# Optimization experiments

Measured on AMD Instinct MI355X. Metric: run time of the kernel, lower is better.

The kernel has to match this reference:

```python
import jax, jax.numpy as jnp
import numpy as np

B, C, L = 8, 256, 2048
D = C // 8  # q/k channel dim = 32


def setup_inputs() -> dict:
    key = jax.random.key(0)
    kx, kq, kk, kv, kg = jax.random.split(key, 5)
    kq1, kq2 = jax.random.split(kq)
    kk1, kk2 = jax.random.split(kk)
    kv1, kv2 = jax.random.split(kv)
    s = 0.05
    return {
        "x": jax.random.normal(kx, (B, C, L), dtype=jnp.float32),
        "Wq": jax.random.normal(kq1, (D, C), dtype=jnp.float32) * s,
        "bq": jax.random.normal(kq2, (D,), dtype=jnp.float32) * s,
        "Wk": jax.random.normal(kk1, (D, C), dtype=jnp.float32) * s,
        "bk": jax.random.normal(kk2, (D,), dtype=jnp.float32) * s,
        "Wv": jax.random.normal(kv1, (C, C), dtype=jnp.float32) * s,
        "bv": jax.random.normal(kv2, (C,), dtype=jnp.float32) * s,
        "gamma": jax.random.normal(kg, (1,), dtype=jnp.float32) * 0.1,
    }


def reference(x, Wq, bq, Wk, bk, Wv, bv, gamma):
    # 1x1 Conv1d == per-position channel matmul
    Q = jnp.einsum("dc,bcl->bld", Wq, x) + bq            # (B, L, D)
    K = jnp.einsum("dc,bcl->bdl", Wk, x) + bk[:, None]   # (B, D, L)
    V = jnp.einsum("oc,bcl->bol", Wv, x) + bv[:, None]   # (B, C, L)
    scale = jnp.float32(1.0 / np.sqrt(D))
    # attn[b, i, j]: softmax over j (keys)
    attn = jax.nn.softmax(jnp.einsum("bid,bdj->bij", Q, K) * scale, axis=-1)
    # out = V @ attn^T : out[b, c, i] = sum_j V[b, c, j] * attn[b, i, j]
    out = jnp.einsum("bcj,bij->bci", V, attn)            # (B, C, L)
    return gamma * out + x
```

## Files before the change

### kernel.cpp

```cpp
#include <hip/hip_runtime.h>
#include <stdint.h>


#define BB 8
#define CC 256
#define LL 2048
#define DD 32

typedef unsigned short u16;
typedef __attribute__((ext_vector_type(8))) short short8;
typedef __attribute__((ext_vector_type(4))) float f32x4;

#define SCALE_LOG2E 0.2550348612f

static __device__ __forceinline__ uint32_t pack2bf16(float hi, float lo) {
    return (__float_as_uint(hi) & 0xFFFF0000u) | (__float_as_uint(lo) >> 16);
}

static __device__ __forceinline__ float fexp2(float v) {
#if __has_builtin(__builtin_amdgcn_exp2f)
    return __builtin_amdgcn_exp2f(v);
#else
    return exp2f(v);
#endif
}

static __device__ __forceinline__ float frcp(float v) {
#if __has_builtin(__builtin_amdgcn_rcpf)
    return __builtin_amdgcn_rcpf(v);
#else
    return 1.0f / v;
#endif
}

__global__ __launch_bounds__(256) void prep_w_kernel(
    const float* __restrict__ Wq, const float* __restrict__ Wk,
    const float* __restrict__ Wv, u16* __restrict__ Wh)
{
    int idx = blockIdx.x * 256 + threadIdx.x;
    int r = idx >> 6;
    int c4 = (idx & 63) << 2;
    const float* src;
    if (r < 32)       src = Wq + (size_t)r * CC + c4;
    else if (r < 64)  src = Wk + (size_t)(r - 32) * CC + c4;
    else              src = Wv + (size_t)(r - 64) * CC + c4;
    float4 v = *(const float4*)src;
    uint2 o;
    o.x = pack2bf16(v.y, v.x);
    o.y = pack2bf16(v.w, v.z);
    *(uint2*)(Wh + (size_t)r * CC + c4) = o;
}

__global__ __launch_bounds__(256) void prep_xt_kernel(
    const float* __restrict__ x, u16* __restrict__ xt)
{
    __shared__ float xs[64 * 65];
    const int blk = blockIdx.x;
    const int b = blk & 7;
    const int t = blk >> 3;
    const int l0 = (t & 31) << 6;
    const int c0 = (t >> 5) << 6;
    const int tid = threadIdx.x;
    const int ln16 = tid & 15;
    const int r0 = tid >> 4;

    const float* xb = x + ((size_t)(b * CC + c0)) * LL + l0;
#pragma unroll
    for (int rr = 0; rr < 4; ++rr) {
        const int c = r0 + rr * 16;
        const float4 v = *(const float4*)(xb + (size_t)c * LL + ln16 * 4);
        float* d = &xs[c * 65 + ln16 * 4];
        d[0] = v.x; d[1] = v.y; d[2] = v.z; d[3] = v.w;
    }
    __syncthreads();
    u16* xo = xt + ((size_t)(b * LL + l0)) * CC + c0;
    const int c4 = ln16 * 4;
#pragma unroll
    for (int rr = 0; rr < 4; ++rr) {
        const int l = r0 + rr * 16;
        const float f0 = xs[(c4 + 0) * 65 + l];
        const float f1 = xs[(c4 + 1) * 65 + l];
        const float f2 = xs[(c4 + 2) * 65 + l];
        const float f3 = xs[(c4 + 3) * 65 + l];
        uint2 o; o.x = pack2bf16(f1, f0); o.y = pack2bf16(f3, f2);
        *(uint2*)(xo + (size_t)l * CC + c4) = o;
    }
}

__global__ __launch_bounds__(256, 4) void proj_kernel(
    const u16* __restrict__ xt, const u16* __restrict__ Wh,
    const float* __restrict__ bq, const float* __restrict__ bk,
    const float* __restrict__ bv,
    u16* __restrict__ Qh, u16* __restrict__ Kth, u16* __restrict__ Vh)
{
    const int blk = blockIdx.x;
    const int b = blk & 7;
    const int t = blk >> 3;
    const int l0 = (t & 63) << 5;
    const int mh = t >> 6;
    const int tid = threadIdx.x;
    const int w = tid >> 6;
    const int lane = tid & 63;
    const int ln = lane & 15;
    const int q = lane >> 4;
    const int wl = w & 1;
    const int wm = w >> 1;
    const int l = l0 + wl * 16 + ln;
    const u16* xrow = xt + ((size_t)(b * LL) + l) * CC;
    const int mbase = mh * 160 + wm * 80;

    f32x4 acc[5];
#pragma unroll
    for (int i = 0; i < 5; ++i) acc[i] = (f32x4){0.f, 0.f, 0.f, 0.f};

#pragma unroll
    for (int c0 = 0; c0 < CC; c0 += 32) {
        const short8 bf = *(const short8*)(xrow + c0 + q * 8);
#pragma unroll
        for (int mt = 0; mt < 5; ++mt) {
            const short8 af = *(const short8*)(Wh + (size_t)(mbase + mt * 16 + ln) * CC + c0 + q * 8);
            acc[mt] = __builtin_amdgcn_mfma_f32_16x16x32_bf16(af, bf, acc[mt], 0, 0, 0);
        }
    }

#pragma unroll
    for (int mt = 0; mt < 5; ++mt) {
        const int rg = mbase + mt * 16 + q * 4;
        if (rg < 32) {
            float v0 = (acc[mt][0] + bq[rg + 0]) * SCALE_LOG2E;
            float v1 = (acc[mt][1] + bq[rg + 1]) * SCALE_LOG2E;
            float v2 = (acc[mt][2] + bq[rg + 2]) * SCALE_LOG2E;
            float v3 = (acc[mt][3] + bq[rg + 3]) * SCALE_LOG2E;
            uint2 o; o.x = pack2bf16(v1, v0); o.y = pack2bf16(v3, v2);
            *(uint2*)(Qh + ((size_t)(b * LL) + l) * DD + rg) = o;
        } else if (rg < 64) {
            const int rk = rg - 32;
            float v0 = acc[mt][0] + bk[rk + 0];
            float v1 = acc[mt][1] + bk[rk + 1];
            float v2 = acc[mt][2] + bk[rk + 2];
            float v3 = acc[mt][3] + bk[rk + 3];
            uint2 o; o.x = pack2bf16(v1, v0); o.y = pack2bf16(v3, v2);
            *(uint2*)(Kth + ((size_t)(b * LL) + l) * DD + rk) = o;
        } else {
            const int cv = rg - 64;
#pragma unroll
            for (int rr = 0; rr < 4; ++rr) {
                const float v = acc[mt][rr] + bv[cv + rr];
                Vh[((size_t)(b * CC) + cv + rr) * LL + l] = (u16)(__float_as_uint(v) >> 16);
            }
        }
    }
}

__global__ __launch_bounds__(512, 2) void attn_kernel(
    const u16* __restrict__ Qh, const u16* __restrict__ Kth,
    const u16* __restrict__ Vh, const float* __restrict__ x,
    const float* __restrict__ gamma, float* __restrict__ out)
{
    __shared__ u16 pbuf[64 * 264];
    __shared__ float lbuf[8 * 64];

    const int blk = blockIdx.x;
    const int b = blk & 7;
    const int i0 = (blk >> 3) << 6;
    const int tid = threadIdx.x;
    const int w = tid >> 6;
    const int lane = tid & 63;
    const int ln = lane & 15;
    const int q = lane >> 4;

    const u16* Qb = Qh + ((size_t)(b * LL) + i0) * DD;
    const u16* Kb = Kth + (size_t)(b * LL) * DD;
    const u16* Vb = Vh + ((size_t)(b * CC) + w * 32) * LL;

    short8 qf[4];
#pragma unroll
    for (int it = 0; it < 4; ++it)
        qf[it] = *(const short8*)(Qb + (size_t)(it * 16 + ln) * DD + q * 8);

    const f32x4 zf = {0.f, 0.f, 0.f, 0.f};
    f32x4 oacc[2][4];
#pragma unroll
    for (int a = 0; a < 2; ++a)
#pragma unroll
        for (int c = 0; c < 4; ++c) oacc[a][c] = zf;
    float lsum[4] = {0.f, 0.f, 0.f, 0.f};

    for (int jm = 0; jm < 8; ++jm) {
        const int j0 = jm * 256;
        const int js = j0 + w * 32;

#pragma unroll
        for (int jt = 0; jt < 2; ++jt) {
            const short8 kf = *(const short8*)(Kb + (size_t)(js + jt * 16 + ln) * DD + q * 8);
#pragma unroll
            for (int it = 0; it < 4; ++it) {
                const f32x4 st = __builtin_amdgcn_mfma_f32_16x16x32_bf16(kf, qf[it], zf, 0, 0, 0);
                const float e0 = fexp2(st[0]), e1 = fexp2(st[1]);
                const float e2 = fexp2(st[2]), e3 = fexp2(st[3]);
                lsum[it] += (e0 + e1) + (e2 + e3);
                uint2 d; d.x = pack2bf16(e1, e0); d.y = pack2bf16(e3, e2);
                *(uint2*)(&pbuf[(it * 16 + ln) * 264 + w * 32 + jt * 16 + q * 4]) = d;
            }
        }
        __syncthreads();

        short8 vf0 = *(const short8*)(Vb + (size_t)(ln) * LL + j0 + q * 8);
        short8 vf1 = *(const short8*)(Vb + (size_t)(16 + ln) * LL + j0 + q * 8);
#pragma unroll
        for (int k = 0; k < 8; ++k) {
            const int kn = ((k + 1) & 7) * 32;
            const short8 vn0 = *(const short8*)(Vb + (size_t)(ln) * LL + j0 + kn + q * 8);
            const short8 vn1 = *(const short8*)(Vb + (size_t)(16 + ln) * LL + j0 + kn + q * 8);
#pragma unroll
            for (int it = 0; it < 4; ++it) {
                const short8 pf = *(const short8*)(&pbuf[(it * 16 + ln) * 264 + k * 32 + q * 8]);
                oacc[0][it] = __builtin_amdgcn_mfma_f32_16x16x32_bf16(vf0, pf, oacc[0][it], 0, 0, 0);
                oacc[1][it] = __builtin_amdgcn_mfma_f32_16x16x32_bf16(vf1, pf, oacc[1][it], 0, 0, 0);
            }
            vf0 = vn0; vf1 = vn1;
        }
        __syncthreads();
    }

#pragma unroll
    for (int it = 0; it < 4; ++it) {
        float s = lsum[it];
        s += __shfl_xor(s, 16);
        s += __shfl_xor(s, 32);
        lsum[it] = s;
    }
    if (q == 0) {
#pragma unroll
        for (int it = 0; it < 4; ++it) lbuf[w * 64 + it * 16 + ln] = lsum[it];
    }
    __syncthreads();

    const float g = gamma[0];
    float linv[4];
#pragma unroll
    for (int it = 0; it < 4; ++it) {
        float s = 0.f;
#pragma unroll
        for (int ww = 0; ww < 8; ++ww) s += lbuf[ww * 64 + it * 16 + ln];
        linv[it] = frcp(s);
    }

#pragma unroll
    for (int ct = 0; ct < 2; ++ct) {
        const int c = w * 32 + ct * 16 + q * 4;
#pragma unroll
        for (int it = 0; it < 4; ++it) {
            const int i = i0 + it * 16 + ln;
#pragma unroll
            for (int r = 0; r < 4; ++r) {
                const size_t idx = ((size_t)(b * CC + c + r)) * LL + i;
                out[idx] = g * (oacc[ct][it][r] * linv[it]) + x[idx];
            }
        }
    }
}

extern "C" void kernel_launch(void* const* d_in, const int* in_sizes, int n_in,
                              void* d_out, int out_size, void* d_ws, size_t ws_size,
                              hipStream_t stream)
{
    const float* x     = (const float*)d_in[0];
    const float* Wq    = (const float*)d_in[1];
    const float* bq    = (const float*)d_in[2];
    const float* Wk    = (const float*)d_in[3];
    const float* bk    = (const float*)d_in[4];
    const float* Wv    = (const float*)d_in[5];
    const float* bv    = (const float*)d_in[6];
    const float* gamma = (const float*)d_in[7];
    float* out = (float*)d_out;

    uint8_t* ws = (uint8_t*)d_ws;
    u16* Wh  = (u16*)(ws + 0x000000);
    u16* xt  = (u16*)(ws + 0x040000);
    u16* Qh  = (u16*)(ws + 0x840000);
    u16* Kth = (u16*)(ws + 0x940000);
    u16* Vh  = (u16*)(ws + 0xA40000);

    prep_w_kernel<<<80, 256, 0, stream>>>(Wq, Wk, Wv, Wh);
    prep_xt_kernel<<<1024, 256, 0, stream>>>(x, xt);
    proj_kernel<<<1024, 256, 0, stream>>>(xt, Wh, bq, bk, bv, Qh, Kth, Vh);
    attn_kernel<<<256, 512, 0, stream>>>(Qh, Kth, Vh, x, gamma, out);
}
```

Before: 157.4 us.

## Fuse x transpose into projection and restructure attention with per-wave P tiles

The separate prep_xt kernel is removed. The projection kernel now loads x tiles directly, converts them to bf16 and transposes them through LDS, which saves a kernel launch and one global write/read pass. The attention kernel now splits its waves into 2 channel groups by 4 key groups, each wave with a private P tile in LDS. This removes the two block-wide barriers per key chunk, at the cost of large per-wave accumulators and a final LDS reduction across key groups. Row sums are now computed twice (once per channel group), so the normalisation applies a factor of 2 to compensate.

Result: faster. 148.9 us (-5.4%).

```diff
diff --git a/kernel.cpp b/kernel.cpp
--- a/kernel.cpp
+++ b/kernel.cpp
@@ -51,63 +51,38 @@
     *(uint2*)(Wh + (size_t)r * CC + c4) = o;
 }
 
-__global__ __launch_bounds__(256) void prep_xt_kernel(
-    const float* __restrict__ x, u16* __restrict__ xt)
-{
-    __shared__ float xs[64 * 65];
-    const int blk = blockIdx.x;
-    const int b = blk & 7;
-    const int t = blk >> 3;
-    const int l0 = (t & 31) << 6;
-    const int c0 = (t >> 5) << 6;
-    const int tid = threadIdx.x;
-    const int ln16 = tid & 15;
-    const int r0 = tid >> 4;
-
-    const float* xb = x + ((size_t)(b * CC + c0)) * LL + l0;
-#pragma unroll
-    for (int rr = 0; rr < 4; ++rr) {
-        const int c = r0 + rr * 16;
-        const float4 v = *(const float4*)(xb + (size_t)c * LL + ln16 * 4);
-        float* d = &xs[c * 65 + ln16 * 4];
-        d[0] = v.x; d[1] = v.y; d[2] = v.z; d[3] = v.w;
-    }
-    __syncthreads();
-    u16* xo = xt + ((size_t)(b * LL + l0)) * CC + c0;
-    const int c4 = ln16 * 4;
-#pragma unroll
-    for (int rr = 0; rr < 4; ++rr) {
-        const int l = r0 + rr * 16;
-        const float f0 = xs[(c4 + 0) * 65 + l];
-        const float f1 = xs[(c4 + 1) * 65 + l];
-        const float f2 = xs[(c4 + 2) * 65 + l];
-        const float f3 = xs[(c4 + 3) * 65 + l];
-        uint2 o; o.x = pack2bf16(f1, f0); o.y = pack2bf16(f3, f2);
-        *(uint2*)(xo + (size_t)l * CC + c4) = o;
-    }
-}
-
-__global__ __launch_bounds__(256, 4) void proj_kernel(
-    const u16* __restrict__ xt, const u16* __restrict__ Wh,
+__global__ __launch_bounds__(512, 2) void proj_kernel(
+    const float* __restrict__ x, const u16* __restrict__ Wh,
     const float* __restrict__ bq, const float* __restrict__ bk,
     const float* __restrict__ bv,
     u16* __restrict__ Qh, u16* __restrict__ Kth, u16* __restrict__ Vh)
 {
+    __shared__ u16 xls[32 * 264];
     const int blk = blockIdx.x;
     const int b = blk & 7;
-    const int t = blk >> 3;
-    const int l0 = (t & 63) << 5;
-    const int mh = t >> 6;
+    const int l0 = (blk >> 3) << 5;
     const int tid = threadIdx.x;
     const int w = tid >> 6;
     const int lane = tid & 63;
     const int ln = lane & 15;
     const int q = lane >> 4;
+
+#pragma unroll
+    for (int cc = 0; cc < 4; ++cc) {
+        const int c = cc * 64 + (tid >> 3);
+        const int l4 = (tid & 7) * 4;
+        const float4 v = *(const float4*)(x + ((size_t)(b * CC + c)) * LL + l0 + l4);
+        xls[(l4 + 0) * 264 + c] = (u16)(__float_as_uint(v.x) >> 16);
+        xls[(l4 + 1) * 264 + c] = (u16)(__float_as_uint(v.y) >> 16);
+        xls[(l4 + 2) * 264 + c] = (u16)(__float_as_uint(v.z) >> 16);
+        xls[(l4 + 3) * 264 + c] = (u16)(__float_as_uint(v.w) >> 16);
+    }
+    __syncthreads();
+
     const int wl = w & 1;
     const int wm = w >> 1;
+    const int mbase = wm * 80;
     const int l = l0 + wl * 16 + ln;
-    const u16* xrow = xt + ((size_t)(b * LL) + l) * CC;
-    const int mbase = mh * 160 + wm * 80;
 
     f32x4 acc[5];
 #pragma unroll
@@ -115,7 +90,7 @@
 
 #pragma unroll
     for (int c0 = 0; c0 < CC; c0 += 32) {
-        const short8 bf = *(const short8*)(xrow + c0 + q * 8);
+        const short8 bf = *(const short8*)(&xls[(wl * 16 + ln) * 264 + c0 + q * 8]);
 #pragma unroll
         for (int mt = 0; mt < 5; ++mt) {
             const short8 af = *(const short8*)(Wh + (size_t)(mbase + mt * 16 + ln) * CC + c0 + q * 8);
@@ -152,12 +127,13 @@
     }
 }
 
-__global__ __launch_bounds__(512, 2) void attn_kernel(
+__global__ __launch_bounds__(512, 1) void attn_kernel(
     const u16* __restrict__ Qh, const u16* __restrict__ Kth,
     const u16* __restrict__ Vh, const float* __restrict__ x,
     const float* __restrict__ gamma, float* __restrict__ out)
 {
-    __shared__ u16 pbuf[64 * 264];
+    __shared__ u16 pbuf[8 * 64 * 40];
+    __shared__ float obuf[256 * 68];
     __shared__ float lbuf[8 * 64];
 
     const int blk = blockIdx.x;
@@ -165,13 +141,16 @@
     const int i0 = (blk >> 3) << 6;
     const int tid = threadIdx.x;
     const int w = tid >> 6;
+    const int wc = w >> 2;
+    const int wj = w & 3;
     const int lane = tid & 63;
     const int ln = lane & 15;
     const int q = lane >> 4;
 
+    u16* pb = pbuf + w * (64 * 40);
     const u16* Qb = Qh + ((size_t)(b * LL) + i0) * DD;
     const u16* Kb = Kth + (size_t)(b * LL) * DD;
-    const u16* Vb = Vh + ((size_t)(b * CC) + w * 32) * LL;
+    const u16* Vb = Vh + ((size_t)(b * CC) + wc * 128) * LL;
 
     short8 qf[4];
 #pragma unroll
@@ -179,20 +158,31 @@
         qf[it] = *(const short8*)(Qb + (size_t)(it * 16 + ln) * DD + q * 8);
 
     const f32x4 zf = {0.f, 0.f, 0.f, 0.f};
-    f32x4 oacc[2][4];
-#pragma unroll
-    for (int a = 0; a < 2; ++a)
+    f32x4 oacc[8][4];
+#pragma unroll
+    for (int a = 0; a < 8; ++a)
 #pragma unroll
         for (int c = 0; c < 4; ++c) oacc[a][c] = zf;
     float lsum[4] = {0.f, 0.f, 0.f, 0.f};
 
-    for (int jm = 0; jm < 8; ++jm) {
-        const int j0 = jm * 256;
-        const int js = j0 + w * 32;
+    int jb = wj * 32;
+    short8 kf0 = *(const short8*)(Kb + (size_t)(jb + ln) * DD + q * 8);
+    short8 kf1 = *(const short8*)(Kb + (size_t)(jb + 16 + ln) * DD + q * 8);
+
+    for (int n = 0; n < 16; ++n) {
+        jb = n * 128 + wj * 32;
+        const int jnx = (n < 15) ? (n + 1) * 128 + wj * 32 : jb;
+
+        short8 vf[8];
+#pragma unroll
+        for (int ct = 0; ct < 8; ++ct)
+            vf[ct] = *(const short8*)(Vb + (size_t)(ct * 16 + ln) * LL + jb + q * 8);
+        const short8 kn0 = *(const short8*)(Kb + (size_t)(jnx + ln) * DD + q * 8);
+        const short8 kn1 = *(const short8*)(Kb + (size_t)(jnx + 16 + ln) * DD + q * 8);
 
 #pragma unroll
         for (int jt = 0; jt < 2; ++jt) {
-            const short8 kf = *(const short8*)(Kb + (size_t)(js + jt * 16 + ln) * DD + q * 8);
+            const short8 kf = jt ? kf1 : kf0;
 #pragma unroll
             for (int it = 0; it < 4; ++it) {
                 const f32x4 st = __builtin_amdgcn_mfma_f32_16x16x32_bf16(kf, qf[it], zf, 0, 0, 0);
@@ -200,27 +190,22 @@
                 const float e2 = fexp2(st[2]), e3 = fexp2(st[3]);
                 lsum[it] += (e0 + e1) + (e2 + e3);
                 uint2 d; d.x = pack2bf16(e1, e0); d.y = pack2bf16(e3, e2);
-                *(uint2*)(&pbuf[(it * 16 + ln) * 264 + w * 32 + jt * 16 + q * 4]) = d;
+                *(uint2*)(&pb[(it * 16 + ln) * 40 + jt * 16 + q * 4]) = d;
             }
         }
-        __syncthreads();
-
-        short8 vf0 = *(const short8*)(Vb + (size_t)(ln) * LL + j0 + q * 8);
-        short8 vf1 = *(const short8*)(Vb + (size_t)(16 + ln) * LL + j0 + q * 8);
-#pragma unroll
-        for (int k = 0; k < 8; ++k) {
-            const int kn = ((k + 1) & 7) * 32;
-            const short8 vn0 = *(const short8*)(Vb + (size_t)(ln) * LL + j0 + kn + q * 8);
-            const short8 vn1 = *(const short8*)(Vb + (size_t)(16 + ln) * LL + j0 + kn + q * 8);
-#pragma unroll
-            for (int it = 0; it < 4; ++it) {
-                const short8 pf = *(const short8*)(&pbuf[(it * 16 + ln) * 264 + k * 32 + q * 8]);
-                oacc[0][it] = __builtin_amdgcn_mfma_f32_16x16x32_bf16(vf0, pf, oacc[0][it], 0, 0, 0);
-                oacc[1][it] = __builtin_amdgcn_mfma_f32_16x16x32_bf16(vf1, pf, oacc[1][it], 0, 0, 0);
-            }
-            vf0 = vn0; vf1 = vn1;
-        }
-        __syncthreads();
+
+        short8 pf[4];
+#pragma unroll
+        for (int it = 0; it < 4; ++it)
+            pf[it] = *(const short8*)(&pb[(it * 16 + ln) * 40 + q * 8]);
+
+#pragma unroll
+        for (int ct = 0; ct < 8; ++ct)
+#pragma unroll
+            for (int it = 0; it < 4; ++it)
+                oacc[ct][it] = __builtin_amdgcn_mfma_f32_16x16x32_bf16(vf[ct], pf[it], oacc[ct][it], 0, 0, 0);
+
+        kf0 = kn0; kf1 = kn1;
     }
 
 #pragma unroll
@@ -234,30 +219,50 @@
 #pragma unroll
         for (int it = 0; it < 4; ++it) lbuf[w * 64 + it * 16 + ln] = lsum[it];
     }
-    __syncthreads();
+
+#pragma unroll
+    for (int p = 0; p < 4; ++p) {
+        if (wj == p) {
+#pragma unroll
+            for (int ct = 0; ct < 8; ++ct)
+#pragma unroll
+                for (int it = 0; it < 4; ++it) {
+                    const int i = it * 16 + ln;
+#pragma unroll
+                    for (int r = 0; r < 4; ++r) {
+                        const int c = wc * 128 + ct * 16 + q * 4 + r;
+                        if (p == 0) obuf[c * 68 + i] = oacc[ct][it][r];
+                        else        obuf[c * 68 + i] += oacc[ct][it][r];
+                    }
+                }
+        }
+        __syncthreads();
+    }
 
     const float g = gamma[0];
-    float linv[4];
-#pragma unroll
-    for (int it = 0; it < 4; ++it) {
-        float s = 0.f;
-#pragma unroll
-        for (int ww = 0; ww < 8; ++ww) s += lbuf[ww * 64 + it * 16 + ln];
-        linv[it] = frcp(s);
-    }
-
-#pragma unroll
-    for (int ct = 0; ct < 2; ++ct) {
-        const int c = w * 32 + ct * 16 + q * 4;
-#pragma unroll
-        for (int it = 0; it < 4; ++it) {
-            const int i = i0 + it * 16 + ln;
-#pragma unroll
-            for (int r = 0; r < 4; ++r) {
-                const size_t idx = ((size_t)(b * CC + c + r)) * LL + i;
-                out[idx] = g * (oacc[ct][it][r] * linv[it]) + x[idx];
-            }
-        }
+    const int i4 = (tid & 15) * 4;
+    float4 sv = {0.f, 0.f, 0.f, 0.f};
+#pragma unroll
+    for (int ww = 0; ww < 8; ++ww) {
+        const float4 lv = *(const float4*)&lbuf[ww * 64 + i4];
+        sv.x += lv.x; sv.y += lv.y; sv.z += lv.z; sv.w += lv.w;
+    }
+    float4 li;
+    li.x = 2.0f * frcp(sv.x); li.y = 2.0f * frcp(sv.y);
+    li.z = 2.0f * frcp(sv.z); li.w = 2.0f * frcp(sv.w);
+
+#pragma unroll
+    for (int cc = 0; cc < 8; ++cc) {
+        const int c = cc * 32 + (tid >> 4);
+        const float4 ov = *(const float4*)&obuf[c * 68 + i4];
+        const size_t idx = ((size_t)(b * CC + c)) * LL + i0 + i4;
+        const float4 xv = *(const float4*)(x + idx);
+        float4 o;
+        o.x = g * (ov.x * li.x) + xv.x;
+        o.y = g * (ov.y * li.y) + xv.y;
+        o.z = g * (ov.z * li.z) + xv.z;
+        o.w = g * (ov.w * li.w) + xv.w;
+        *(float4*)(out + idx) = o;
     }
 }
 
@@ -277,13 +282,11 @@
 
     uint8_t* ws = (uint8_t*)d_ws;
     u16* Wh  = (u16*)(ws + 0x000000);
-    u16* xt  = (u16*)(ws + 0x040000);
-    u16* Qh  = (u16*)(ws + 0x840000);
-    u16* Kth = (u16*)(ws + 0x940000);
-    u16* Vh  = (u16*)(ws + 0xA40000);
+    u16* Qh  = (u16*)(ws + 0x040000);
+    u16* Kth = (u16*)(ws + 0x140000);
+    u16* Vh  = (u16*)(ws + 0x240000);
 
     prep_w_kernel<<<80, 256, 0, stream>>>(Wq, Wk, Wv, Wh);
-    prep_xt_kernel<<<1024, 256, 0, stream>>>(x, xt);
-    proj_kernel<<<1024, 256, 0, stream>>>(xt, Wh, bq, bk, bv, Qh, Kth, Vh);
+    proj_kernel<<<512, 512, 0, stream>>>(x, Wh, bq, bk, bv, Qh, Kth, Vh);
     attn_kernel<<<256, 512, 0, stream>>>(Qh, Kth, Vh, x, gamma, out);
 }
```
